# Performance work log

Measured on AMD Instinct MI355X. Metric: run time of the kernel, lower is better.

## Reference

```python
import jax, jax.numpy as jnp
import numpy as np

N_NODES = 100000
N_EDGES = 1600000


def gcn_conv(h_in, src, dst, norm, W, b, n_nodes):
    # h_in: [N, Fin]; src/dst: [E'] (self-loops included); norm: [E']
    h = h_in @ W                                    # [N, Fout]
    msg = h[src] * norm[:, None]                    # gather + scale
    out = jax.ops.segment_sum(msg, dst, num_segments=n_nodes)
    return out + b


def _with_self_loops_and_norm(edge_index, n_nodes):
    loop = jnp.arange(n_nodes, dtype=edge_index.dtype)
    src = jnp.concatenate([edge_index[0], loop])
    dst = jnp.concatenate([edge_index[1], loop])
    deg = jax.ops.segment_sum(jnp.ones_like(dst, dtype=jnp.float32), dst,
                              num_segments=n_nodes)
    dinv = jnp.where(deg > 0, jax.lax.rsqrt(deg), 0.0)
    norm = dinv[src] * dinv[dst]                    # [E+N]
    return src, dst, norm


def setup_inputs() -> dict:
    key = jax.random.key(0)
    k1, k2, k3, k4 = jax.random.split(key, 4)
    x = jax.random.normal(k1, (N_NODES, 256), dtype=jnp.float32)
    edge_index = jax.random.randint(k2, (2, N_EDGES), 0, N_NODES, dtype=jnp.int64)
    W1 = jax.random.normal(k3, (256, 128), dtype=jnp.float32) * (1.0 / np.sqrt(256))
    b1 = jnp.zeros((128,), dtype=jnp.float32)
    W2 = jax.random.normal(k4, (128, 40), dtype=jnp.float32) * (1.0 / np.sqrt(128))
    b2 = jnp.zeros((40,), dtype=jnp.float32)
    return {"x": x, "edge_index": edge_index, "W1": W1, "b1": b1, "W2": W2, "b2": b2}


def reference(x, edge_index, W1, b1, W2, b2):
    n_nodes = x.shape[0]
    src, dst, norm = _with_self_loops_and_norm(edge_index, n_nodes)
    h = jax.nn.relu(gcn_conv(x, src, dst, norm, W1, b1, n_nodes))
    # dropout p=0.5 is identity in eval mode
    h = gcn_conv(h, src, dst, norm, W2, b2, n_nodes)
    return jax.nn.log_softmax(h, axis=-1)
```

## Files before the change

### kernel.cpp

```cpp
#include <hip/hip_runtime.h>
#include <hip/hip_bf16.h>
#include <math.h>

#define FIN 256
#define FMID 128
#define FOUT 40

typedef __attribute__((ext_vector_type(8))) short bf16x8;
typedef __attribute__((ext_vector_type(4))) float f32x4;

__device__ __forceinline__ short f2b(float f) {
    __hip_bfloat16 h = __float2bfloat16(f);
    return *reinterpret_cast<short*>(&h);
}

__device__ __forceinline__ float blo(uint b) { union { uint u; float f; } v; v.u = b << 16; return v.f; }
__device__ __forceinline__ float bhi(uint b) { union { uint u; float f; } v; v.u = b & 0xFFFF0000u; return v.f; }

__global__ __launch_bounds__(256) void k_count_pos(const int* __restrict__ dst,
                                                   int* __restrict__ counts,
                                                   int* __restrict__ pos, int E) {
    int e = blockIdx.x * 256 + threadIdx.x;
    if (e < E) pos[e] = atomicAdd(&counts[dst[e]], 1);
}

__global__ __launch_bounds__(256) void k_alloc(int* __restrict__ counts,
                                               int* __restrict__ start,
                                               float* __restrict__ dinv,
                                               int* __restrict__ gcnt,
                                               int* __restrict__ ebuf, int n) {
    __shared__ int s[256];
    __shared__ int base_s;
    int t = threadIdx.x;
    int i = blockIdx.x * 256 + t;
    int c = (i < n) ? counts[i] + 1 : 0;
    s[t] = c;
    __syncthreads();
    #pragma unroll
    for (int off = 1; off < 256; off <<= 1) {
        int v = (t >= off) ? s[t - off] : 0;
        __syncthreads();
        s[t] += v;
        __syncthreads();
    }
    if (t == 255) base_s = atomicAdd(gcnt, s[255]);
    __syncthreads();
    if (i < n) {
        int st = base_s + s[t] - c;
        start[i]  = st;
        dinv[i]   = rsqrtf((float)c);
        counts[i] = c;
        ebuf[st]  = i;
    }
}

__global__ __launch_bounds__(256) void k_fill2(const int* __restrict__ src,
                                               const int* __restrict__ dst,
                                               const int* __restrict__ start,
                                               const int* __restrict__ pos,
                                               int* __restrict__ ebuf, int E) {
    int e = blockIdx.x * 256 + threadIdx.x;
    if (e >= E) return;
    int d = dst[e];
    ebuf[start[d] + 1 + pos[e]] = src[e];
}

__global__ __launch_bounds__(256) void k_prepw1(const float* __restrict__ W1,
                                                short* __restrict__ w1t) {
    int t = blockIdx.x * 256 + threadIdx.x;
    if (t >= FIN * FMID) return;
    int k = t >> 7;
    int n = t & 127;
    w1t[n * FIN + k] = f2b(W1[t]);
}

__global__ __launch_bounds__(256) void k_gemm1b(const float* __restrict__ A,
                                                const short* __restrict__ w1t,
                                                ushort* __restrict__ Cb, int M) {
    __shared__ short Bs[FMID * FIN];

    const int t = threadIdx.x;
    {
        int c  = t & 31;
        int r0 = t >> 5;
        #pragma unroll
        for (int p = 0; p < 16; ++p) {
            int n = r0 + p * 8;
            int dst = n * FIN + ((c * 8) ^ ((n & 7) << 3));
            *(bf16x8*)(&Bs[dst]) = *(const bf16x8*)(&w1t[n * FIN + c * 8]);
        }
    }
    __syncthreads();

    const int wid  = t >> 6;
    const int lane = t & 63;
    const int l15  = lane & 15;
    const int kg   = lane >> 4;
    const int mbase = blockIdx.x * 128 + wid * 32;

    f32x4 acc[2][8] = {};

    for (int ks = 0; ks < 8; ++ks) {
        const int k0 = ks * 32;
        bf16x8 bf[8];
        #pragma unroll
        for (int ct = 0; ct < 8; ++ct) {
            int n = ct * 16 + l15;
            bf[ct] = *(const bf16x8*)(&Bs[n * FIN + ((k0 + kg * 8) ^ ((n & 7) << 3))]);
        }
        #pragma unroll
        for (int rt = 0; rt < 2; ++rt) {
            int row = mbase + rt * 16 + l15;
            bf16x8 af = {0, 0, 0, 0, 0, 0, 0, 0};
            if (row < M) {
                const float* ap = &A[(size_t)row * FIN + k0 + kg * 8];
                float4 a0 = *(const float4*)(ap);
                float4 a1 = *(const float4*)(ap + 4);
                af[0] = f2b(a0.x); af[1] = f2b(a0.y);
                af[2] = f2b(a0.z); af[3] = f2b(a0.w);
                af[4] = f2b(a1.x); af[5] = f2b(a1.y);
                af[6] = f2b(a1.z); af[7] = f2b(a1.w);
            }
            #pragma unroll
            for (int ct = 0; ct < 8; ++ct)
                acc[rt][ct] = __builtin_amdgcn_mfma_f32_16x16x32_bf16(
                    af, bf[ct], acc[rt][ct], 0, 0, 0);
        }
    }

    #pragma unroll
    for (int rt = 0; rt < 2; ++rt) {
        #pragma unroll
        for (int r = 0; r < 4; ++r) {
            int row = mbase + rt * 16 + kg * 4 + r;
            if (row < M) {
                #pragma unroll
                for (int ct = 0; ct < 8; ++ct)
                    Cb[(size_t)row * FMID + ct * 16 + l15] =
                        (ushort)f2b(acc[rt][ct][r]);
            }
        }
    }
}

__global__ __launch_bounds__(256) void k_agg1(const ushort* __restrict__ hb,
                                              const int* __restrict__ ebuf,
                                              const int* __restrict__ start,
                                              const int* __restrict__ cnt,
                                              const float* __restrict__ dinv,
                                              const float* __restrict__ b1,
                                              float* __restrict__ out, int Nn) {
    int node = __builtin_amdgcn_readfirstlane(blockIdx.x * 4 + (threadIdx.x >> 6));
    int lane = threadIdx.x & 63;
    if (node >= Nn) return;
    int rs = start[node];
    int n  = cnt[node];
    float di = dinv[node];
    float2 acc = make_float2(0.f, 0.f);
    const int off2 = lane * 2;
    int k = 0;
    for (; k + 4 <= n; k += 4) {
        int s0 = ebuf[rs + k + 0];
        int s1 = ebuf[rs + k + 1];
        int s2 = ebuf[rs + k + 2];
        int s3 = ebuf[rs + k + 3];
        float w0 = dinv[s0], w1 = dinv[s1], w2 = dinv[s2], w3 = dinv[s3];
        uint v0 = *(const uint*)(&hb[(size_t)s0 * FMID + off2]);
        uint v1 = *(const uint*)(&hb[(size_t)s1 * FMID + off2]);
        uint v2 = *(const uint*)(&hb[(size_t)s2 * FMID + off2]);
        uint v3 = *(const uint*)(&hb[(size_t)s3 * FMID + off2]);
        acc.x += w0 * blo(v0) + w1 * blo(v1) + w2 * blo(v2) + w3 * blo(v3);
        acc.y += w0 * bhi(v0) + w1 * bhi(v1) + w2 * bhi(v2) + w3 * bhi(v3);
    }
    for (; k < n; ++k) {
        int s   = ebuf[rs + k];
        float w = dinv[s];
        uint v  = *(const uint*)(&hb[(size_t)s * FMID + off2]);
        acc.x += w * blo(v);
        acc.y += w * bhi(v);
    }
    float2 bv = *(const float2*)(&b1[off2]);
    acc.x = fmaxf(di * acc.x + bv.x, 0.f);
    acc.y = fmaxf(di * acc.y + bv.y, 0.f);
    *(float2*)(&out[(size_t)node * FMID + off2]) = acc;
}

#define G2_PAD 132
__global__ __launch_bounds__(256) void k_gemm2(const float* __restrict__ A,
                                               const float* __restrict__ W2,
                                               float* __restrict__ C, int M) {
    __shared__ float w2t[FOUT * G2_PAD];
    __shared__ float As[64 * G2_PAD];

    const int t = threadIdx.x;
    const int block_row = blockIdx.x * 64;

    for (int idx = t; idx < FMID * FOUT; idx += 256) {
        int k = idx / FOUT;
        int j = idx - k * FOUT;
        w2t[j * G2_PAD + k] = W2[idx];
    }

    {
        int r  = t >> 5;
        int c4 = (t & 31) * 4;
        #pragma unroll
        for (int p = 0; p < 8; ++p) {
            int row = block_row + r + p * 8;
            float4 v = (row < M) ? *(const float4*)(&A[(size_t)row * FMID + c4])
                                 : make_float4(0.f, 0.f, 0.f, 0.f);
            *(float4*)(&As[(r + p * 8) * G2_PAD + c4]) = v;
        }
    }
    __syncthreads();

    const int cg    = t & 7;
    const int rg    = t >> 3;
    const int cbase = cg * 5;
    const float* a0p = &As[(rg * 2 + 0) * G2_PAD];
    const float* a1p = &As[(rg * 2 + 1) * G2_PAD];

    float acc0[5] = {}, acc1[5] = {};
    #pragma unroll 4
    for (int k = 0; k < FMID; k += 4) {
        float4 a0 = *(const float4*)(a0p + k);
        float4 a1 = *(const float4*)(a1p + k);
        #pragma unroll
        for (int j = 0; j < 5; ++j) {
            float4 w = *(const float4*)(&w2t[(cbase + j) * G2_PAD + k]);
            acc0[j] += a0.x * w.x + a0.y * w.y + a0.z * w.z + a0.w * w.w;
            acc1[j] += a1.x * w.x + a1.y * w.y + a1.z * w.z + a1.w * w.w;
        }
    }

    int row0 = block_row + rg * 2;
    if (row0 < M) {
        #pragma unroll
        for (int j = 0; j < 5; ++j) C[(size_t)row0 * FOUT + cbase + j] = acc0[j];
    }
    if (row0 + 1 < M) {
        #pragma unroll
        for (int j = 0; j < 5; ++j) C[(size_t)(row0 + 1) * FOUT + cbase + j] = acc1[j];
    }
}

__global__ __launch_bounds__(256) void k_agg2(const float* __restrict__ h,
                                              const int* __restrict__ ebuf,
                                              const int* __restrict__ start,
                                              const int* __restrict__ cnt,
                                              const float* __restrict__ dinv,
                                              const float* __restrict__ b2,
                                              float* __restrict__ out, int Nn) {
    int node = __builtin_amdgcn_readfirstlane(blockIdx.x * 4 + (threadIdx.x >> 6));
    int lane = threadIdx.x & 63;
    if (node >= Nn) return;
    int rs = start[node];
    int n  = cnt[node];
    float di = dinv[node];
    float acc = 0.f;
    bool active = (lane < FOUT);
    int lidx = active ? lane : 0;
    int k = 0;
    for (; k + 4 <= n; k += 4) {
        int s0 = ebuf[rs + k + 0];
        int s1 = ebuf[rs + k + 1];
        int s2 = ebuf[rs + k + 2];
        int s3 = ebuf[rs + k + 3];
        float w0 = dinv[s0], w1 = dinv[s1], w2 = dinv[s2], w3 = dinv[s3];
        float v0 = h[(size_t)s0 * FOUT + lidx];
        float v1 = h[(size_t)s1 * FOUT + lidx];
        float v2 = h[(size_t)s2 * FOUT + lidx];
        float v3 = h[(size_t)s3 * FOUT + lidx];
        acc += w0 * v0 + w1 * v1 + w2 * v2 + w3 * v3;
    }
    for (; k < n; ++k) {
        int s   = ebuf[rs + k];
        acc += dinv[s] * h[(size_t)s * FOUT + lidx];
    }
    float v = active ? di * acc + b2[lane] : -INFINITY;
    float m = v;
    #pragma unroll
    for (int off = 32; off >= 1; off >>= 1) m = fmaxf(m, __shfl_xor(m, off));
    float e = active ? expf(v - m) : 0.f;
    float ssum = e;
    #pragma unroll
    for (int off = 32; off >= 1; off >>= 1) ssum += __shfl_xor(ssum, off);
    if (active) out[(size_t)node * FOUT + lane] = v - m - logf(ssum);
}

extern "C" void kernel_launch(void* const* d_in, const int* in_sizes, int n_in,
                              void* d_out, int out_size, void* d_ws, size_t ws_size,
                              hipStream_t stream) {
    const float* x  = (const float*)d_in[0];
    const int*   ei = (const int*)d_in[1];
    const float* W1 = (const float*)d_in[2];
    const float* b1 = (const float*)d_in[3];
    const float* W2 = (const float*)d_in[4];
    const float* b2 = (const float*)d_in[5];

    const int N = in_sizes[0] / FIN;
    const int E = in_sizes[1] / 2;
    float* out = (float*)d_out;

    ushort* h1b   = (ushort*)d_ws;
    float*  agg1  = (float*)(h1b + (size_t)N * FMID);
    float*  dinv  = agg1 + (size_t)N * FMID;
    int*    counts= (int*)(dinv + N);
    int*    start = counts + N;
    int*    gcnt  = start + N;
    int*    ebuf  = gcnt + 64;
    short*  w1t   = (short*)(ebuf + (size_t)(E + N));
    int*    pos   = (int*)(w1t + FIN * FMID);
    float*  h2    = (float*)h1b;

    const int* srcp = ei;
    const int* dstp = ei + E;

    k_prepw1<<<(FIN * FMID + 255) / 256, 256, 0, stream>>>(W1, w1t);

    hipMemsetAsync(gcnt, 0, sizeof(int), stream);
    hipMemsetAsync(counts, 0, (size_t)N * sizeof(int), stream);
    k_count_pos<<<(E + 255) / 256, 256, 0, stream>>>(dstp, counts, pos, E);
    k_alloc    <<<(N + 255) / 256, 256, 0, stream>>>(counts, start, dinv, gcnt, ebuf, N);
    k_fill2    <<<(E + 255) / 256, 256, 0, stream>>>(srcp, dstp, start, pos, ebuf, E);

    k_gemm1b<<<(N + 127) / 128, 256, 0, stream>>>(x, w1t, h1b, N);
    k_agg1  <<<(N + 3) / 4, 256, 0, stream>>>(h1b, ebuf, start, counts, dinv, b1, agg1, N);

    k_gemm2<<<(N + 63) / 64, 256, 0, stream>>>(agg1, W2, h2, N);
    k_agg2 <<<(N + 3) / 4, 256, 0, stream>>>(h2, ebuf, start, counts, dinv, b2, out, N);
}
```

Before: 475.9 us.

## Fold source-node dinv scaling into GEMM epilogues and batch edge kernels four-per-thread

The per-source normalization dinv[src] is applied once per row in the GEMM1 and GEMM2 epilogues, so the aggregation kernels no longer gather dinv for every edge and only sum pre-scaled rows. The edge-processing kernels (count/pos and fill) now handle four edges per thread with grouped loads and atomics to expose more memory-level parallelism. Scaling before the bf16 rounding in GEMM1 slightly changes numerics.

```diff
diff --git a/kernel.cpp b/kernel.cpp
--- a/kernel.cpp
+++ b/kernel.cpp
@@ -20,8 +20,22 @@
 __global__ __launch_bounds__(256) void k_count_pos(const int* __restrict__ dst,
                                                    int* __restrict__ counts,
                                                    int* __restrict__ pos, int E) {
-    int e = blockIdx.x * 256 + threadIdx.x;
-    if (e < E) pos[e] = atomicAdd(&counts[dst[e]], 1);
+    int tid    = blockIdx.x * 256 + threadIdx.x;
+    int stride = gridDim.x * 256;
+    int e0 = tid, e1 = tid + stride, e2 = tid + 2 * stride, e3 = tid + 3 * stride;
+    int d0 = (e0 < E) ? dst[e0] : 0;
+    int d1 = (e1 < E) ? dst[e1] : 0;
+    int d2 = (e2 < E) ? dst[e2] : 0;
+    int d3 = (e3 < E) ? dst[e3] : 0;
+    int p0, p1, p2, p3;
+    if (e0 < E) p0 = atomicAdd(&counts[d0], 1);
+    if (e1 < E) p1 = atomicAdd(&counts[d1], 1);
+    if (e2 < E) p2 = atomicAdd(&counts[d2], 1);
+    if (e3 < E) p3 = atomicAdd(&counts[d3], 1);
+    if (e0 < E) pos[e0] = p0;
+    if (e1 < E) pos[e1] = p1;
+    if (e2 < E) pos[e2] = p2;
+    if (e3 < E) pos[e3] = p3;
 }
 
 __global__ __launch_bounds__(256) void k_alloc(int* __restrict__ counts,
@@ -59,10 +73,30 @@
                                                const int* __restrict__ start,
                                                const int* __restrict__ pos,
                                                int* __restrict__ ebuf, int E) {
-    int e = blockIdx.x * 256 + threadIdx.x;
-    if (e >= E) return;
-    int d = dst[e];
-    ebuf[start[d] + 1 + pos[e]] = src[e];
+    int tid    = blockIdx.x * 256 + threadIdx.x;
+    int stride = gridDim.x * 256;
+    int e0 = tid, e1 = tid + stride, e2 = tid + 2 * stride, e3 = tid + 3 * stride;
+    bool v0 = e0 < E, v1 = e1 < E, v2 = e2 < E, v3 = e3 < E;
+    int d0 = v0 ? dst[e0] : 0;
+    int d1 = v1 ? dst[e1] : 0;
+    int d2 = v2 ? dst[e2] : 0;
+    int d3 = v3 ? dst[e3] : 0;
+    int p0 = v0 ? pos[e0] : 0;
+    int p1 = v1 ? pos[e1] : 0;
+    int p2 = v2 ? pos[e2] : 0;
+    int p3 = v3 ? pos[e3] : 0;
+    int s0 = v0 ? src[e0] : 0;
+    int s1 = v1 ? src[e1] : 0;
+    int s2 = v2 ? src[e2] : 0;
+    int s3 = v3 ? src[e3] : 0;
+    int st0 = v0 ? start[d0] : 0;
+    int st1 = v1 ? start[d1] : 0;
+    int st2 = v2 ? start[d2] : 0;
+    int st3 = v3 ? start[d3] : 0;
+    if (v0) ebuf[st0 + 1 + p0] = s0;
+    if (v1) ebuf[st1 + 1 + p1] = s1;
+    if (v2) ebuf[st2 + 1 + p2] = s2;
+    if (v3) ebuf[st3 + 1 + p3] = s3;
 }
 
 __global__ __launch_bounds__(256) void k_prepw1(const float* __restrict__ W1,
@@ -76,6 +110,7 @@
 
 __global__ __launch_bounds__(256) void k_gemm1b(const float* __restrict__ A,
                                                 const short* __restrict__ w1t,
+                                                const float* __restrict__ dinv,
                                                 ushort* __restrict__ Cb, int M) {
     __shared__ short Bs[FMID * FIN];
 
@@ -134,10 +169,11 @@
         for (int r = 0; r < 4; ++r) {
             int row = mbase + rt * 16 + kg * 4 + r;
             if (row < M) {
+                float sc = dinv[row];
                 #pragma unroll
                 for (int ct = 0; ct < 8; ++ct)
                     Cb[(size_t)row * FMID + ct * 16 + l15] =
-                        (ushort)f2b(acc[rt][ct][r]);
+                        (ushort)f2b(acc[rt][ct][r] * sc);
             }
         }
     }
@@ -164,20 +200,18 @@
         int s1 = ebuf[rs + k + 1];
         int s2 = ebuf[rs + k + 2];
         int s3 = ebuf[rs + k + 3];
-        float w0 = dinv[s0], w1 = dinv[s1], w2 = dinv[s2], w3 = dinv[s3];
         uint v0 = *(const uint*)(&hb[(size_t)s0 * FMID + off2]);
         uint v1 = *(const uint*)(&hb[(size_t)s1 * FMID + off2]);
         uint v2 = *(const uint*)(&hb[(size_t)s2 * FMID + off2]);
         uint v3 = *(const uint*)(&hb[(size_t)s3 * FMID + off2]);
-        acc.x += w0 * blo(v0) + w1 * blo(v1) + w2 * blo(v2) + w3 * blo(v3);
-        acc.y += w0 * bhi(v0) + w1 * bhi(v1) + w2 * bhi(v2) + w3 * bhi(v3);
+        acc.x += blo(v0) + blo(v1) + blo(v2) + blo(v3);
+        acc.y += bhi(v0) + bhi(v1) + bhi(v2) + bhi(v3);
     }
     for (; k < n; ++k) {
         int s   = ebuf[rs + k];
-        float w = dinv[s];
         uint v  = *(const uint*)(&hb[(size_t)s * FMID + off2]);
-        acc.x += w * blo(v);
-        acc.y += w * bhi(v);
+        acc.x += blo(v);
+        acc.y += bhi(v);
     }
     float2 bv = *(const float2*)(&b1[off2]);
     acc.x = fmaxf(di * acc.x + bv.x, 0.f);
@@ -188,6 +222,7 @@
 #define G2_PAD 132
 __global__ __launch_bounds__(256) void k_gemm2(const float* __restrict__ A,
                                                const float* __restrict__ W2,
+                                               const float* __restrict__ dinv,
                                                float* __restrict__ C, int M) {
     __shared__ float w2t[FOUT * G2_PAD];
     __shared__ float As[64 * G2_PAD];
@@ -235,12 +270,14 @@
 
     int row0 = block_row + rg * 2;
     if (row0 < M) {
-        #pragma unroll
-        for (int j = 0; j < 5; ++j) C[(size_t)row0 * FOUT + cbase + j] = acc0[j];
+        float sc = dinv[row0];
+        #pragma unroll
+        for (int j = 0; j < 5; ++j) C[(size_t)row0 * FOUT + cbase + j] = acc0[j] * sc;
     }
     if (row0 + 1 < M) {
-        #pragma unroll
-        for (int j = 0; j < 5; ++j) C[(size_t)(row0 + 1) * FOUT + cbase + j] = acc1[j];
+        float sc = dinv[row0 + 1];
+        #pragma unroll
+        for (int j = 0; j < 5; ++j) C[(size_t)(row0 + 1) * FOUT + cbase + j] = acc1[j] * sc;
     }
 }
 
@@ -266,16 +303,15 @@
         int s1 = ebuf[rs + k + 1];
         int s2 = ebuf[rs + k + 2];
         int s3 = ebuf[rs + k + 3];
-        float w0 = dinv[s0], w1 = dinv[s1], w2 = dinv[s2], w3 = dinv[s3];
         float v0 = h[(size_t)s0 * FOUT + lidx];
         float v1 = h[(size_t)s1 * FOUT + lidx];
         float v2 = h[(size_t)s2 * FOUT + lidx];
         float v3 = h[(size_t)s3 * FOUT + lidx];
-        acc += w0 * v0 + w1 * v1 + w2 * v2 + w3 * v3;
+        acc += v0 + v1 + v2 + v3;
     }
     for (; k < n; ++k) {
-        int s   = ebuf[rs + k];
-        acc += dinv[s] * h[(size_t)s * FOUT + lidx];
+        int s = ebuf[rs + k];
+        acc += h[(size_t)s * FOUT + lidx];
     }
     float v = active ? di * acc + b2[lane] : -INFINITY;
     float m = v;
@@ -320,13 +356,13 @@
 
     hipMemsetAsync(gcnt, 0, sizeof(int), stream);
     hipMemsetAsync(counts, 0, (size_t)N * sizeof(int), stream);
-    k_count_pos<<<(E + 255) / 256, 256, 0, stream>>>(dstp, counts, pos, E);
+    k_count_pos<<<(E + 1023) / 1024, 256, 0, stream>>>(dstp, counts, pos, E);
     k_alloc    <<<(N + 255) / 256, 256, 0, stream>>>(counts, start, dinv, gcnt, ebuf, N);
-    k_fill2    <<<(E + 255) / 256, 256, 0, stream>>>(srcp, dstp, start, pos, ebuf, E);
-
-    k_gemm1b<<<(N + 127) / 128, 256, 0, stream>>>(x, w1t, h1b, N);
+    k_fill2    <<<(E + 1023) / 1024, 256, 0, stream>>>(srcp, dstp, start, pos, ebuf, E);
+
+    k_gemm1b<<<(N + 127) / 128, 256, 0, stream>>>(x, w1t, dinv, h1b, N);
     k_agg1  <<<(N + 3) / 4, 256, 0, stream>>>(h1b, ebuf, start, counts, dinv, b1, agg1, N);
 
-    k_gemm2<<<(N + 63) / 64, 256, 0, stream>>>(agg1, W2, h2, N);
+    k_gemm2<<<(N + 63) / 64, 256, 0, stream>>>(agg1, W2, dinv, h2, N);
     k_agg2 <<<(N + 3) / 4, 256, 0, stream>>>(h2, ebuf, start, counts, dinv, b2, out, N);
 }
```

Result: no change. 468.1 us (-1.6%).
